# Optimization experiments

Hardware: AMD Instinct MI355X
Metric: run time of the kernel (lower is better)

Reference implementation:

```python
import jax, jax.numpy as jnp
import numpy as np

D_MODEL = 512
NUM_HEADS = 8
HEAD_DIM = D_MODEL // NUM_HEADS
NEG_INF = -1e9


def setup_inputs() -> dict:
    key = jax.random.key(0)
    ks = jax.random.split(key, 12)
    B, S = 4, 2048
    std = 1.0 / np.sqrt(D_MODEL)
    inp = {
        "query": jax.random.normal(ks[0], (B, S, D_MODEL), jnp.float32),
        "key": jax.random.normal(ks[1], (B, S, D_MODEL), jnp.float32),
        "value": jax.random.normal(ks[2], (B, S, D_MODEL), jnp.float32),
        "mask": jax.random.randint(ks[3], (B, 1, S, S), 0, 2, jnp.int32),
        "Wq": jax.random.normal(ks[4], (D_MODEL, D_MODEL), jnp.float32) * std,
        "bq": jnp.zeros((D_MODEL,), jnp.float32),
        "Wk": jax.random.normal(ks[5], (D_MODEL, D_MODEL), jnp.float32) * std,
        "bk": jnp.zeros((D_MODEL,), jnp.float32),
        "Wv": jax.random.normal(ks[6], (D_MODEL, D_MODEL), jnp.float32) * std,
        "bv": jnp.zeros((D_MODEL,), jnp.float32),
        "Wo": jax.random.normal(ks[7], (D_MODEL, D_MODEL), jnp.float32) * std,
        "bo": jnp.zeros((D_MODEL,), jnp.float32),
    }
    return inp


def _split_heads(x):
    B, S, _ = x.shape
    return x.reshape(B, S, NUM_HEADS, HEAD_DIM).transpose(0, 2, 1, 3)  # [B,H,S,Dh]


def reference(query, key, value, mask, Wq, bq, Wk, bk, Wv, bv, Wo, bo):
    B, S, _ = query.shape
    q = _split_heads(query @ Wq + bq)
    k = _split_heads(key @ Wk + bk)
    v = _split_heads(value @ Wv + bv)
    # scores: [B,H,S,S]
    scores = jnp.einsum("bhqd,bhkd->bhqk", q, k) / jnp.sqrt(jnp.float32(HEAD_DIM))
    scores = jnp.where(mask == 0, jnp.float32(NEG_INF), scores)
    attn = jax.nn.softmax(scores, axis=-1)  # dropout p=0 -> identity
    out = jnp.einsum("bhqk,bhkd->bhqd", attn, v)
    out = out.transpose(0, 2, 1, 3).reshape(B, S, D_MODEL)
    return out @ Wo + bo
```

## Files before the change

kernel.cpp:

```cpp
#include <hip/hip_runtime.h>

typedef unsigned short u16;
typedef __attribute__((ext_vector_type(4))) float f32x4;
typedef __attribute__((ext_vector_type(8))) short s16x8;
typedef __attribute__((ext_vector_type(4))) unsigned short u16x4;

__device__ __forceinline__ u16 f2bf(float f) {
    union { float f; unsigned u; } v; v.f = f;
    unsigned r = v.u + 0x7fffu + ((v.u >> 16) & 1u);
    return (u16)(r >> 16);
}
__device__ __forceinline__ float bf2f(u16 h) {
    union { unsigned u; float f; } v; v.u = ((unsigned)h) << 16;
    return v.f;
}
__device__ __forceinline__ float fexp2(float x) {
#if __has_builtin(__builtin_amdgcn_exp2f)
    return __builtin_amdgcn_exp2f(x);
#else
    return exp2f(x);
#endif
}
__device__ __forceinline__ void gload16(const void* g, void* lds_uniform) {
    __builtin_amdgcn_global_load_lds(
        (const __attribute__((address_space(1))) void*)g,
        (__attribute__((address_space(3))) void*)lds_uniform, 16, 0, 0);
}
__device__ __forceinline__ f32x4 mfma16(s16x8 a, s16x8 b, f32x4 c) {
    return __builtin_amdgcn_mfma_f32_16x16x32_bf16(a, b, c, 0, 0, 0);
}

__global__ void prep(const float4* __restrict__ q, const float4* __restrict__ k,
                     const float4* __restrict__ v, u16x4* __restrict__ qkv,
                     const float* __restrict__ Wq, const float* __restrict__ Wk,
                     const float* __restrict__ Wv, const float* __restrict__ Wo,
                     u16* __restrict__ WqT, u16* __restrict__ WkT,
                     u16* __restrict__ WvT, u16* __restrict__ WoT,
                     const int* __restrict__ mask, unsigned* __restrict__ bits) {
    __shared__ float tile[32][33];
    const int bid = blockIdx.x, tid = threadIdx.x;
    if (bid < 12288) {
        int i = bid * 256 + tid;
        int sel = i >> 20, j = i & 0xFFFFF;
        const float4* in = (sel == 0) ? q : (sel == 1) ? k : v;
        float4 f = in[j];
        u16x4 o;
        o[0] = f2bf(f.x); o[1] = f2bf(f.y); o[2] = f2bf(f.z); o[3] = f2bf(f.w);
        qkv[i] = o;
    } else if (bid < 13312) {
        int idx = bid - 12288;
        int bz = idx >> 8, rem = idx & 255, by = rem >> 4, bx = rem & 15;
        const float* W; u16* T;
        switch (bz) {
            case 0: W = Wq; T = WqT; break;
            case 1: W = Wk; T = WkT; break;
            case 2: W = Wv; T = WvT; break;
            default: W = Wo; T = WoT; break;
        }
        const int tx = tid & 31, ty = tid >> 5;
        const int k0 = by * 32, n0 = bx * 32;
#pragma unroll
        for (int r = 0; r < 32; r += 8) tile[ty + r][tx] = W[(k0 + ty + r) * 512 + n0 + tx];
        __syncthreads();
#pragma unroll
        for (int r = 0; r < 32; r += 8) T[(n0 + ty + r) * 512 + k0 + tx] = f2bf(tile[tx][ty + r]);
    } else {
        int i = (bid - 13312) * 256 + tid;
        int m = mask[i];
        unsigned long long bal = __ballot(m != 0);
        if ((tid & 63) == 0) {
            uint2 w2; w2.x = (unsigned)bal; w2.y = (unsigned)(bal >> 32);
            *(uint2*)&bits[i >> 5] = w2;
        }
    }
}

template <int BM, int BIAS_ROW, int OUT_F32>
__global__ __launch_bounds__(256, 4) void gemm_bt(
    const u16* __restrict__ A, const u16* __restrict__ Bt0, const u16* __restrict__ Bt1,
    const float* __restrict__ bias0, const float* __restrict__ bias1,
    void* __restrict__ Cout, int M, int N, int K, int ysplit) {
    constexpr int MR = BM / 32;
    const u16* Bt = (blockIdx.y < (unsigned)ysplit) ? Bt0 : Bt1;
    const float* bias = (blockIdx.y < (unsigned)ysplit) ? bias0 : bias1;
    __shared__ u16 As[BM * 32];
    __shared__ u16 Bs[64 * 32];
    const int t = threadIdx.x, l = t & 63, w = t >> 6;
    const int lr = l & 15, lg = l >> 4;
    const int m0 = blockIdx.y * BM, n0 = blockIdx.x * 64;
    const int wr = w >> 1, wc = w & 1;
    f32x4 acc[MR][2] = {};
    const int ar = t >> 2, ac = (t & 3) * 8;

    for (int kk = 0; kk < K; kk += 32) {
        __syncthreads();
        gload16(A + (m0 + ar) * K + kk + ac, As + w * 512);
        if (BM == 128)
            gload16(A + (m0 + 64 + ar) * K + kk + ac, As + 2048 + w * 512);
        gload16(Bt + (n0 + ar) * K + kk + ac, Bs + w * 512);
        __syncthreads();
        s16x8 af[MR], bfr[2];
#pragma unroll
        for (int m = 0; m < MR; ++m)
            af[m] = *(const s16x8*)&As[(wr * (BM / 2) + m * 16 + lr) * 32 + lg * 8];
#pragma unroll
        for (int n = 0; n < 2; ++n)
            bfr[n] = *(const s16x8*)&Bs[(wc * 32 + n * 16 + lr) * 32 + lg * 8];
#pragma unroll
        for (int m = 0; m < MR; ++m)
#pragma unroll
            for (int n = 0; n < 2; ++n) acc[m][n] = mfma16(af[m], bfr[n], acc[m][n]);
    }

#pragma unroll
    for (int n = 0; n < 2; ++n) {
        const int cg = n0 + wc * 32 + n * 16 + lr;
        const float bcol = BIAS_ROW ? 0.f : bias[cg];
#pragma unroll
        for (int m = 0; m < MR; ++m) {
            const int rbase = m0 + wr * (BM / 2) + m * 16 + lg * 4;
#pragma unroll
            for (int j = 0; j < 4; ++j) {
                const int rg = rbase + j;
                float val = acc[m][n][j] + (BIAS_ROW ? bias[rg] : bcol);
                if (OUT_F32) ((float*)Cout)[(size_t)rg * N + cg] = val;
                else         ((u16*)Cout)[(size_t)rg * N + cg] = f2bf(val);
            }
        }
    }
}

__global__ __launch_bounds__(256, 4) void attn_fwd(
    const u16* __restrict__ Qp, const u16* __restrict__ Kp,
    const u16* __restrict__ Vt, const unsigned* __restrict__ mbits,
    u16* __restrict__ AO) {
    constexpr int S = 2048;
    const int qt = blockIdx.x, bh = blockIdx.y;
    const int b = bh >> 3, h = bh & 7;
    const int t = threadIdx.x, l = t & 63, w = t >> 6;
    const int lr = l & 15, lg = l >> 4;

    __shared__ u16 Ks[64 * 64];
    __shared__ u16 Vs[64 * 64];
    __shared__ u16 Ps[4][16 * 64];

    const int q0 = qt * 64 + w * 16;
    const int bS = b * S;

    s16x8 qf[2];
#pragma unroll
    for (int ks = 0; ks < 2; ++ks) {
        s16x8 v = *(const s16x8*)&Qp[(bS + q0 + lr) * 512 + h * 64 + ks * 32 + lg * 8];
#pragma unroll
        for (int j = 0; j < 8; ++j) v[j] = (short)f2bf(bf2f((u16)v[j]) * 0.1803368851f);
        qf[ks] = v;
    }

    f32x4 po[4] = {};
    float lrun[4] = {0.f, 0.f, 0.f, 0.f};

    const int kc0 = t, kc1 = 256 + t;
    const int krow0 = kc0 >> 3, kcol0 = ((kc0 & 7) ^ (krow0 & 7)) * 8;
    const int krow1 = kc1 >> 3, kcol1 = ((kc1 & 7) ^ (krow1 & 7)) * 8;

    for (int kt0 = 0; kt0 < S; kt0 += 64) {
        __syncthreads();
        gload16(&Kp[(bS + kt0 + krow0) * 512 + h * 64 + kcol0], &Ks[w * 512]);
        gload16(&Kp[(bS + kt0 + krow1) * 512 + h * 64 + kcol1], &Ks[2048 + w * 512]);
        gload16(&Vt[(h * 64 + krow0) * (4 * S) + bS + kt0 + kcol0], &Vs[w * 512]);
        gload16(&Vt[(h * 64 + krow1) * (4 * S) + bS + kt0 + kcol1], &Vs[2048 + w * 512]);

        uint2 mw[4];
#pragma unroll
        for (int jj = 0; jj < 4; ++jj)
            mw[jj] = *(const uint2*)&mbits[(bS + q0 + lg * 4 + jj) * 64 + (kt0 >> 5)];
        __syncthreads();

        f32x4 sc[4];
#pragma unroll
        for (int nk = 0; nk < 4; ++nk) sc[nk] = f32x4{0.f, 0.f, 0.f, 0.f};
#pragma unroll
        for (int nk = 0; nk < 4; ++nk) {
            const int ktc = nk * 16 + lr;
            const int sw = (ktc & 7) << 4;
            s16x8 k0 = *(const s16x8*)((const char*)Ks + ((ktc * 128 + lg * 16) ^ sw));
            s16x8 k1 = *(const s16x8*)((const char*)Ks + ((ktc * 128 + 64 + lg * 16) ^ sw));
            sc[nk] = mfma16(qf[0], k0, sc[nk]);
            sc[nk] = mfma16(qf[1], k1, sc[nk]);
        }

#pragma unroll
        for (int nk = 0; nk < 4; ++nk) {
            const unsigned bp = ((nk & 1) << 4) + lr;
#pragma unroll
            for (int jj = 0; jj < 4; ++jj) {
                const unsigned word = (nk >> 1) ? mw[jj].y : mw[jj].x;
                const float s = ((word >> bp) & 1u) ? sc[nk][jj] : -1e9f;
                sc[nk][jj] = fexp2(s);
            }
        }
#pragma unroll
        for (int jj = 0; jj < 4; ++jj)
            lrun[jj] += (sc[0][jj] + sc[1][jj]) + (sc[2][jj] + sc[3][jj]);

#pragma unroll
        for (int nk = 0; nk < 4; ++nk) {
            const int ktc = nk * 16 + lr;
#pragma unroll
            for (int jj = 0; jj < 4; ++jj) {
                const int qloc = lg * 4 + jj;
                const int byte = (qloc * 128 + ktc * 2) ^ ((qloc & 7) << 4);
                *(u16*)((char*)&Ps[w][0] + byte) = f2bf(sc[nk][jj]);
            }
        }

        s16x8 pa[2];
#pragma unroll
        for (int k2 = 0; k2 < 2; ++k2) {
            const int byte = (lr * 128 + k2 * 64 + lg * 16) ^ ((lr & 7) << 4);
            pa[k2] = *(const s16x8*)((const char*)&Ps[w][0] + byte);
        }

#pragma unroll
        for (int dn = 0; dn < 4; ++dn) {
            const int d = dn * 16 + lr;
            const int sw = (d & 7) << 4;
            s16x8 v0 = *(const s16x8*)((const char*)Vs + ((d * 128 + lg * 16) ^ sw));
            s16x8 v1 = *(const s16x8*)((const char*)Vs + ((d * 128 + 64 + lg * 16) ^ sw));
            po[dn] = mfma16(pa[0], v0, po[dn]);
            po[dn] = mfma16(pa[1], v1, po[dn]);
        }
    }

#pragma unroll
    for (int jj = 0; jj < 4; ++jj) {
        float s = lrun[jj];
        s += __shfl_xor(s, 1);
        s += __shfl_xor(s, 2);
        s += __shfl_xor(s, 4);
        s += __shfl_xor(s, 8);
        const float inv = 1.f / s;
        const int q = q0 + lg * 4 + jj;
#pragma unroll
        for (int dn = 0; dn < 4; ++dn)
            AO[(bS + q) * 512 + h * 64 + dn * 16 + lr] = f2bf(po[dn][jj] * inv);
    }
}

extern "C" void kernel_launch(void* const* d_in, const int* in_sizes, int n_in,
                              void* d_out, int out_size, void* d_ws, size_t ws_size,
                              hipStream_t stream) {
    (void)in_sizes; (void)n_in; (void)out_size; (void)ws_size;
    const float* query = (const float*)d_in[0];
    const float* key   = (const float*)d_in[1];
    const float* value = (const float*)d_in[2];
    const int*   mask  = (const int*)d_in[3];
    const float* Wq = (const float*)d_in[4];
    const float* bq = (const float*)d_in[5];
    const float* Wk = (const float*)d_in[6];
    const float* bk = (const float*)d_in[7];
    const float* Wv = (const float*)d_in[8];
    const float* bv = (const float*)d_in[9];
    const float* Wo = (const float*)d_in[10];
    const float* bo = (const float*)d_in[11];

    char* ws = (char*)d_ws;
    const size_t MB = 1ull << 20;
    u16* qb  = (u16*)(ws);
    u16* vb  = (u16*)(ws + 16 * MB);
    u16* WqT = (u16*)(ws + 24 * MB);
    u16* WkT = (u16*)(ws + 24 * MB + 512 * 1024);
    u16* WvT = (u16*)(ws + 25 * MB);
    u16* WoT = (u16*)(ws + 25 * MB + 512 * 1024);
    unsigned* mb = (unsigned*)(ws + 26 * MB);
    u16* Qp = (u16*)(ws + 28 * MB);
    u16* Vt = (u16*)(ws + 44 * MB);
    u16* AO = (u16*)(ws + 52 * MB);

    prep<<<78848, 256, 0, stream>>>((const float4*)query, (const float4*)key,
                                    (const float4*)value, (u16x4*)qb,
                                    Wq, Wk, Wv, Wo, WqT, WkT, WvT, WoT, mask, mb);

    gemm_bt<128, 0, 0><<<dim3(8, 128), 256, 0, stream>>>(qb, WqT, WkT, bq, bk, Qp,
                                                         16384, 512, 512, 64);
    gemm_bt<64, 1, 0><<<dim3(128, 8), 256, 0, stream>>>(WvT, vb, vb, bv, bv, Vt,
                                                        512, 8192, 512, 999);

    attn_fwd<<<dim3(32, 32), 256, 0, stream>>>(Qp, Qp + 8192 * 512, Vt, mb, AO);

    gemm_bt<64, 0, 1><<<dim3(8, 128), 256, 0, stream>>>(AO, WoT, WoT, bo, bo,
                                                        (float*)d_out, 8192, 512, 512, 999);
}
```

Measured before the change: 156.3 us.

## Double-buffer K/V tiles in attention and fold query scaling into projection GEMM

The attention kernel now prefetches the next K/V tile and mask words into a second LDS buffer while computing on the current one, dropping one barrier per iteration. The softmax scale for Q moves into the projection GEMM epilogue through a new per-split scale argument, so the attention prologue no longer rescales Q. The change also adds s_setprio around the MFMA blocks and swaps the manual bf16 rounding for the HIP intrinsic. Doubling K/V LDS raises shared-memory use per block, which may lower occupancy.

```diff
diff --git a/kernel.cpp b/kernel.cpp
--- a/kernel.cpp
+++ b/kernel.cpp
@@ -1,4 +1,5 @@
 #include <hip/hip_runtime.h>
+#include <hip/hip_bf16.h>
 
 typedef unsigned short u16;
 typedef __attribute__((ext_vector_type(4))) float f32x4;
@@ -10,9 +11,9 @@
     unsigned r = v.u + 0x7fffu + ((v.u >> 16) & 1u);
     return (u16)(r >> 16);
 }
-__device__ __forceinline__ float bf2f(u16 h) {
-    union { unsigned u; float f; } v; v.u = ((unsigned)h) << 16;
-    return v.f;
+__device__ __forceinline__ u16 f2bfh(float f) {
+    __hip_bfloat16 h = __float2bfloat16(f);
+    return *reinterpret_cast<u16*>(&h);
 }
 __device__ __forceinline__ float fexp2(float x) {
 #if __has_builtin(__builtin_amdgcn_exp2f)
@@ -79,10 +80,12 @@
 __global__ __launch_bounds__(256, 4) void gemm_bt(
     const u16* __restrict__ A, const u16* __restrict__ Bt0, const u16* __restrict__ Bt1,
     const float* __restrict__ bias0, const float* __restrict__ bias1,
-    void* __restrict__ Cout, int M, int N, int K, int ysplit) {
+    void* __restrict__ Cout, int M, int N, int K, int ysplit,
+    float scale0, float scale1) {
     constexpr int MR = BM / 32;
     const u16* Bt = (blockIdx.y < (unsigned)ysplit) ? Bt0 : Bt1;
     const float* bias = (blockIdx.y < (unsigned)ysplit) ? bias0 : bias1;
+    const float scale = (blockIdx.y < (unsigned)ysplit) ? scale0 : scale1;
     __shared__ u16 As[BM * 32];
     __shared__ u16 Bs[64 * 32];
     const int t = threadIdx.x, l = t & 63, w = t >> 6;
@@ -122,7 +125,7 @@
 #pragma unroll
             for (int j = 0; j < 4; ++j) {
                 const int rg = rbase + j;
-                float val = acc[m][n][j] + (BIAS_ROW ? bias[rg] : bcol);
+                float val = (acc[m][n][j] + (BIAS_ROW ? bias[rg] : bcol)) * scale;
                 if (OUT_F32) ((float*)Cout)[(size_t)rg * N + cg] = val;
                 else         ((u16*)Cout)[(size_t)rg * N + cg] = f2bf(val);
             }
@@ -140,8 +143,8 @@
     const int t = threadIdx.x, l = t & 63, w = t >> 6;
     const int lr = l & 15, lg = l >> 4;
 
-    __shared__ u16 Ks[64 * 64];
-    __shared__ u16 Vs[64 * 64];
+    __shared__ u16 Ks[2][64 * 64];
+    __shared__ u16 Vs[2][64 * 64];
     __shared__ u16 Ps[4][16 * 64];
 
     const int q0 = qt * 64 + w * 16;
@@ -149,12 +152,8 @@
 
     s16x8 qf[2];
 #pragma unroll
-    for (int ks = 0; ks < 2; ++ks) {
-        s16x8 v = *(const s16x8*)&Qp[(bS + q0 + lr) * 512 + h * 64 + ks * 32 + lg * 8];
-#pragma unroll
-        for (int j = 0; j < 8; ++j) v[j] = (short)f2bf(bf2f((u16)v[j]) * 0.1803368851f);
-        qf[ks] = v;
-    }
+    for (int ks = 0; ks < 2; ++ks)
+        qf[ks] = *(const s16x8*)&Qp[(bS + q0 + lr) * 512 + h * 64 + ks * 32 + lg * 8];
 
     f32x4 po[4] = {};
     float lrun[4] = {0.f, 0.f, 0.f, 0.f};
@@ -163,31 +162,48 @@
     const int krow0 = kc0 >> 3, kcol0 = ((kc0 & 7) ^ (krow0 & 7)) * 8;
     const int krow1 = kc1 >> 3, kcol1 = ((kc1 & 7) ^ (krow1 & 7)) * 8;
 
-    for (int kt0 = 0; kt0 < S; kt0 += 64) {
+#define STAGE(nb, kt0)                                                              \
+    do {                                                                            \
+        gload16(&Kp[(bS + (kt0) + krow0) * 512 + h * 64 + kcol0], &Ks[nb][w * 512]);\
+        gload16(&Kp[(bS + (kt0) + krow1) * 512 + h * 64 + kcol1], &Ks[nb][2048 + w * 512]);\
+        gload16(&Vt[(h * 64 + krow0) * (4 * S) + bS + (kt0) + kcol0], &Vs[nb][w * 512]);\
+        gload16(&Vt[(h * 64 + krow1) * (4 * S) + bS + (kt0) + kcol1], &Vs[nb][2048 + w * 512]);\
+    } while (0)
+
+    uint2 mw[4], mwn[4];
+    STAGE(0, 0);
+#pragma unroll
+    for (int jj = 0; jj < 4; ++jj)
+        mw[jj] = *(const uint2*)&mbits[(bS + q0 + lg * 4 + jj) * 64];
+#pragma unroll
+    for (int jj = 0; jj < 4; ++jj) mwn[jj] = mw[jj];
+
+    for (int it = 0; it < 32; ++it) {
+        const int cur = it & 1;
         __syncthreads();
-        gload16(&Kp[(bS + kt0 + krow0) * 512 + h * 64 + kcol0], &Ks[w * 512]);
-        gload16(&Kp[(bS + kt0 + krow1) * 512 + h * 64 + kcol1], &Ks[2048 + w * 512]);
-        gload16(&Vt[(h * 64 + krow0) * (4 * S) + bS + kt0 + kcol0], &Vs[w * 512]);
-        gload16(&Vt[(h * 64 + krow1) * (4 * S) + bS + kt0 + kcol1], &Vs[2048 + w * 512]);
-
-        uint2 mw[4];
-#pragma unroll
-        for (int jj = 0; jj < 4; ++jj)
-            mw[jj] = *(const uint2*)&mbits[(bS + q0 + lg * 4 + jj) * 64 + (kt0 >> 5)];
-        __syncthreads();
+        if (it + 1 < 32) {
+            STAGE(cur ^ 1, (it + 1) * 64);
+#pragma unroll
+            for (int jj = 0; jj < 4; ++jj)
+                mwn[jj] = *(const uint2*)&mbits[(bS + q0 + lg * 4 + jj) * 64 + ((it + 1) << 1)];
+        }
+        const u16* Kc = Ks[cur];
+        const u16* Vc = Vs[cur];
 
         f32x4 sc[4];
 #pragma unroll
         for (int nk = 0; nk < 4; ++nk) sc[nk] = f32x4{0.f, 0.f, 0.f, 0.f};
+        __builtin_amdgcn_s_setprio(1);
 #pragma unroll
         for (int nk = 0; nk < 4; ++nk) {
             const int ktc = nk * 16 + lr;
             const int sw = (ktc & 7) << 4;
-            s16x8 k0 = *(const s16x8*)((const char*)Ks + ((ktc * 128 + lg * 16) ^ sw));
-            s16x8 k1 = *(const s16x8*)((const char*)Ks + ((ktc * 128 + 64 + lg * 16) ^ sw));
+            s16x8 k0 = *(const s16x8*)((const char*)Kc + ((ktc * 128 + lg * 16) ^ sw));
+            s16x8 k1 = *(const s16x8*)((const char*)Kc + ((ktc * 128 + 64 + lg * 16) ^ sw));
             sc[nk] = mfma16(qf[0], k0, sc[nk]);
             sc[nk] = mfma16(qf[1], k1, sc[nk]);
         }
+        __builtin_amdgcn_s_setprio(0);
 
 #pragma unroll
         for (int nk = 0; nk < 4; ++nk) {
@@ -210,7 +226,7 @@
             for (int jj = 0; jj < 4; ++jj) {
                 const int qloc = lg * 4 + jj;
                 const int byte = (qloc * 128 + ktc * 2) ^ ((qloc & 7) << 4);
-                *(u16*)((char*)&Ps[w][0] + byte) = f2bf(sc[nk][jj]);
+                *(u16*)((char*)&Ps[w][0] + byte) = f2bfh(sc[nk][jj]);
             }
         }
 
@@ -221,16 +237,22 @@
             pa[k2] = *(const s16x8*)((const char*)&Ps[w][0] + byte);
         }
 
+        __builtin_amdgcn_s_setprio(1);
 #pragma unroll
         for (int dn = 0; dn < 4; ++dn) {
             const int d = dn * 16 + lr;
             const int sw = (d & 7) << 4;
-            s16x8 v0 = *(const s16x8*)((const char*)Vs + ((d * 128 + lg * 16) ^ sw));
-            s16x8 v1 = *(const s16x8*)((const char*)Vs + ((d * 128 + 64 + lg * 16) ^ sw));
+            s16x8 v0 = *(const s16x8*)((const char*)Vc + ((d * 128 + lg * 16) ^ sw));
+            s16x8 v1 = *(const s16x8*)((const char*)Vc + ((d * 128 + 64 + lg * 16) ^ sw));
             po[dn] = mfma16(pa[0], v0, po[dn]);
             po[dn] = mfma16(pa[1], v1, po[dn]);
         }
-    }
+        __builtin_amdgcn_s_setprio(0);
+
+#pragma unroll
+        for (int jj = 0; jj < 4; ++jj) mw[jj] = mwn[jj];
+    }
+#undef STAGE
 
 #pragma unroll
     for (int jj = 0; jj < 4; ++jj) {
@@ -243,7 +265,7 @@
         const int q = q0 + lg * 4 + jj;
 #pragma unroll
         for (int dn = 0; dn < 4; ++dn)
-            AO[(bS + q) * 512 + h * 64 + dn * 16 + lr] = f2bf(po[dn][jj] * inv);
+            AO[(bS + q) * 512 + h * 64 + dn * 16 + lr] = f2bfh(po[dn][jj] * inv);
     }
 }
 
@@ -281,13 +303,13 @@
                                     (const float4*)value, (u16x4*)qb,
                                     Wq, Wk, Wv, Wo, WqT, WkT, WvT, WoT, mask, mb);
 
-    gemm_bt<128, 0, 0><<<dim3(8, 128), 256, 0, stream>>>(qb, WqT, WkT, bq, bk, Qp,
-                                                         16384, 512, 512, 64);
-    gemm_bt<64, 1, 0><<<dim3(128, 8), 256, 0, stream>>>(WvT, vb, vb, bv, bv, Vt,
-                                                        512, 8192, 512, 999);
+    gemm_bt<128, 0, 0><<<dim3(8, 128), 256, 0, stream>>>(
+        qb, WqT, WkT, bq, bk, Qp, 16384, 512, 512, 64, 0.18033688f, 1.0f);
+    gemm_bt<64, 1, 0><<<dim3(128, 8), 256, 0, stream>>>(
+        WvT, vb, vb, bv, bv, Vt, 512, 8192, 512, 999, 1.0f, 1.0f);
 
     attn_fwd<<<dim3(32, 32), 256, 0, stream>>>(Qp, Qp + 8192 * 512, Vt, mb, AO);
 
-    gemm_bt<64, 0, 1><<<dim3(8, 128), 256, 0, stream>>>(AO, WoT, WoT, bo, bo,
-                                                        (float*)d_out, 8192, 512, 512, 999);
-}
+    gemm_bt<64, 0, 1><<<dim3(8, 128), 256, 0, stream>>>(
+        AO, WoT, WoT, bo, bo, (float*)d_out, 8192, 512, 512, 999, 1.0f, 1.0f);
+}
```

Result: no change. 157.0 us (+0.5%).
